# Kernel tuning notes

Hardware: AMD Instinct MI355X
Metric: run time of the kernel (lower is better)

Reference implementation:

```python
import jax, jax.numpy as jnp
import numpy as np
import math

N_EMBD = 1024
N_HEAD = 16
B, T, T_PLAN = 2, 2048, 512
EPS = 1e-5


def _layernorm(x, g, b):
    m = jnp.mean(x, axis=-1, keepdims=True)
    v = jnp.mean(jnp.square(x - m), axis=-1, keepdims=True)
    return (x - m) * jax.lax.rsqrt(v + EPS) * g + b


def setup_inputs() -> dict:
    key = jax.random.key(0)
    ks = jax.random.split(key, 16)
    C = N_EMBD
    s = 0.02
    inp = {
        "x": jax.random.normal(ks[0], (B, T, C), jnp.float32),
        "plan_hidden": jax.random.normal(ks[1], (B, T_PLAN, C), jnp.float32),
        "ln1_g": jnp.ones((C,), jnp.float32), "ln1_b": jnp.zeros((C,), jnp.float32),
        # weights stored as [in, out] (torch Linear applies x @ W.T)
        "c_attn_w": s * jax.random.normal(ks[2], (C, 3 * C), jnp.float32),
        "c_attn_b": jnp.zeros((3 * C,), jnp.float32),
        "attn_proj_w": s * jax.random.normal(ks[3], (C, C), jnp.float32),
        "attn_proj_b": jnp.zeros((C,), jnp.float32),
        "ln2_g": jnp.ones((C,), jnp.float32), "ln2_b": jnp.zeros((C,), jnp.float32),
        "q_w": s * jax.random.normal(ks[4], (C, C), jnp.float32), "q_b": jnp.zeros((C,), jnp.float32),
        "k_w": s * jax.random.normal(ks[5], (C, C), jnp.float32), "k_b": jnp.zeros((C,), jnp.float32),
        "v_w": s * jax.random.normal(ks[6], (C, C), jnp.float32), "v_b": jnp.zeros((C,), jnp.float32),
        "ca_proj_w": s * jax.random.normal(ks[7], (C, C), jnp.float32),
        "ca_proj_b": jnp.zeros((C,), jnp.float32),
        "ln3_g": jnp.ones((C,), jnp.float32), "ln3_b": jnp.zeros((C,), jnp.float32),
        "fc_w": s * jax.random.normal(ks[8], (C, 4 * C), jnp.float32),
        "fc_b": jnp.zeros((4 * C,), jnp.float32),
        "mlp_proj_w": s * jax.random.normal(ks[9], (4 * C, C), jnp.float32),
        "mlp_proj_b": jnp.zeros((C,), jnp.float32),
    }
    return inp


def _split_heads(t, n_head):  # [B,T,C] -> [B,H,T,D]
    Bs, Ts, Cs = t.shape
    return t.reshape(Bs, Ts, n_head, Cs // n_head).transpose(0, 2, 1, 3)


def _merge_heads(t):  # [B,H,T,D] -> [B,T,C]
    Bs, H, Ts, D = t.shape
    return t.transpose(0, 2, 1, 3).reshape(Bs, Ts, H * D)


def _self_attn(x, c_attn_w, c_attn_b, proj_w, proj_b):
    Bs, Ts, C = x.shape
    qkv = x @ c_attn_w + c_attn_b
    q, k, v = jnp.split(qkv, 3, axis=-1)
    q, k, v = (_split_heads(t, N_HEAD) for t in (q, k, v))
    scale = 1.0 / math.sqrt(C // N_HEAD)
    att = jnp.einsum("bhqd,bhkd->bhqk", q, k) * scale
    mask = jnp.tril(jnp.ones((Ts, Ts), bool))
    att = jnp.where(mask, att, -jnp.inf)
    att = jax.nn.softmax(att, axis=-1)
    y = jnp.einsum("bhqk,bhkd->bhqd", att, v)
    return _merge_heads(y) @ proj_w + proj_b


def _cross_attn(x, plan, q_w, q_b, k_w, k_b, v_w, v_b, proj_w, proj_b):
    C = x.shape[-1]
    q = _split_heads(x @ q_w + q_b, N_HEAD)
    k = _split_heads(plan @ k_w + k_b, N_HEAD)
    v = _split_heads(plan @ v_w + v_b, N_HEAD)
    scale = 1.0 / math.sqrt(C // N_HEAD)
    att = jax.nn.softmax(jnp.einsum("bhqd,bhkd->bhqk", q, k) * scale, axis=-1)
    y = jnp.einsum("bhqk,bhkd->bhqd", att, v)
    return _merge_heads(y) @ proj_w + proj_b


def reference(x, plan_hidden, ln1_g, ln1_b, c_attn_w, c_attn_b, attn_proj_w, attn_proj_b,
              ln2_g, ln2_b, q_w, q_b, k_w, k_b, v_w, v_b, ca_proj_w, ca_proj_b,
              ln3_g, ln3_b, fc_w, fc_b, mlp_proj_w, mlp_proj_b):
    x = x + _self_attn(_layernorm(x, ln1_g, ln1_b), c_attn_w, c_attn_b, attn_proj_w, attn_proj_b)
    x = x + _cross_attn(_layernorm(x, ln2_g, ln2_b), plan_hidden,
                        q_w, q_b, k_w, k_b, v_w, v_b, ca_proj_w, ca_proj_b)
    h = _layernorm(x, ln3_g, ln3_b)
    h = jax.nn.gelu(h @ fc_w + fc_b, approximate=False) @ mlp_proj_w + mlp_proj_b
    return x + h
```

## Files before the change

kernel.cpp:

```cpp
#include <hip/hip_runtime.h>
#include <stdint.h>

typedef __bf16 bf16;
typedef __bf16 bf16x4 __attribute__((ext_vector_type(4)));
typedef __bf16 bf16x8 __attribute__((ext_vector_type(8)));
typedef float  f32x4  __attribute__((ext_vector_type(4)));

#define DEVI __device__ __forceinline__

DEVI void gll16(const void* g, void* l) {
  __builtin_amdgcn_global_load_lds(
      (const __attribute__((address_space(1))) void*)g,
      (__attribute__((address_space(3))) void*)l,
      16, 0, 0);
}

DEVI f32x4 mfma16(bf16x8 a, bf16x8 b, f32x4 c) {
  return __builtin_amdgcn_mfma_f32_16x16x32_bf16(a, b, c, 0, 0, 0);
}

DEVI void wt_body(char* arena, const float* __restrict__ W, bf16* __restrict__ WT,
                  int K, int N, int bx, int by, int tid) {
  float (*t)[65] = reinterpret_cast<float(*)[65]>(arena);
  int bn = bx * 64, bk = by * 64;
  int tx = tid & 63, ty = tid >> 6;
#pragma unroll
  for (int i = 0; i < 16; ++i)
    t[ty + i * 4][tx] = W[(size_t)(bk + ty + i * 4) * N + bn + tx];
  __syncthreads();
#pragma unroll
  for (int i = 0; i < 16; ++i)
    WT[(size_t)(bn + ty + i * 4) * K + bk + tx] = (bf16)t[tx][ty + i * 4];
}

DEVI void ln_body(char* arena, const float* __restrict__ x, const float* __restrict__ g,
                  const float* __restrict__ b, bf16* __restrict__ out, int row, int tid) {
  float* ps  = (float*)arena;
  float* psq = ps + 4;
  f32x4 v = ((const f32x4*)(x + (size_t)row * 1024))[tid];
  float s = v[0] + v[1] + v[2] + v[3];
  float sq = v[0]*v[0] + v[1]*v[1] + v[2]*v[2] + v[3]*v[3];
#pragma unroll
  for (int m = 1; m < 64; m <<= 1) {
    s  += __shfl_xor(s, m, 64);
    sq += __shfl_xor(sq, m, 64);
  }
  int w = tid >> 6;
  if ((tid & 63) == 0) { ps[w] = s; psq[w] = sq; }
  __syncthreads();
  s  = ps[0] + ps[1] + ps[2] + ps[3];
  sq = psq[0] + psq[1] + psq[2] + psq[3];
  float mean = s * (1.f / 1024.f);
  float rs = rsqrtf(sq * (1.f / 1024.f) - mean * mean + 1e-5f);
  f32x4 gv = ((const f32x4*)g)[tid];
  f32x4 bv = ((const f32x4*)b)[tid];
  bf16x4 o;
#pragma unroll
  for (int i = 0; i < 4; ++i) o[i] = (bf16)((v[i] - mean) * rs * gv[i] + bv[i]);
  ((bf16x4*)(out + (size_t)row * 1024))[tid] = o;
}

__global__ __launch_bounds__(256)
void k_ln(const float* __restrict__ x, const float* __restrict__ g,
          const float* __restrict__ b, bf16* __restrict__ out) {
  __shared__ __align__(16) char arena[64];
  ln_body(arena, x, g, b, out, blockIdx.x, threadIdx.x);
}

__global__ __launch_bounds__(256)
void mega_misc(const float* __restrict__ x, const float* __restrict__ g,
               const float* __restrict__ b, bf16* __restrict__ out,
               const float* __restrict__ W, bf16* __restrict__ WT,
               const float* __restrict__ plan, bf16* __restrict__ planb,
               const float* __restrict__ kb, const float* __restrict__ vb,
               float* __restrict__ biaskv) {
  __shared__ __align__(16) char arena[16640];
  const int bid = blockIdx.x, tid = threadIdx.x;
  if (bid < 4096) {
    ln_body(arena, x, g, b, out, bid, tid);
  } else if (bid < 4864) {
    int wid = bid - 4096;
    wt_body(arena, W, WT, 1024, 3072, wid % 48, wid / 48, tid);
  } else if (bid < 5888) {
    int i = (bid - 4864) * 256 + tid;
    f32x4 v = ((const f32x4*)plan)[i];
    bf16x4 o;
    o[0] = (bf16)v[0]; o[1] = (bf16)v[1]; o[2] = (bf16)v[2]; o[3] = (bf16)v[3];
    ((bf16x4*)planb)[i] = o;
  } else {
    int i = (bid - 5888) * 256 + tid;
    biaskv[i] = i < 1024 ? kb[i] : vb[i - 1024];
  }
}

template <int EPI>
DEVI void gemm_s_body(char* arena, const bf16* __restrict__ A, const bf16* __restrict__ BT,
                      const float* __restrict__ bias, void* __restrict__ Cout,
                      int M, int N, int K, const float* __restrict__ Xres,
                      int nwg, int bid) {
  char (*SA)[8192]  = reinterpret_cast<char(*)[8192]>(arena);
  char (*SB)[16384] = reinterpret_cast<char(*)[16384]>(arena + 16384);
  const int tid = threadIdx.x;
  const int lane = tid & 63;
  const int w = tid >> 6;
  const int wr = w >> 1, wc = w & 1;
  const int lr = lane & 15, lg = lane >> 4;
  const int nk = K >> 6;

  const int q = nwg >> 3, r = nwg & 7;
  const int xcd = bid & 7, loc = bid >> 3;
  const int wg = (xcd < r ? xcd * (q + 1) : r * (q + 1) + (xcd - r) * q) + loc;
  const int gy = M >> 6;
  const int m0 = (wg % gy) << 6, n0 = (wg / gy) << 7;

  const int c8 = tid & 7;
  const int hrb = tid >> 3;
  auto stgA = [&](int buf, int ktc) {
#pragma unroll
    for (int i = 0; i < 2; ++i) {
      int hr = i * 32 + hrb;
      const bf16* s = A + (size_t)(m0 + hr) * K + ((size_t)ktc << 6) + ((c8 ^ (hr & 7)) << 3);
      gll16(s, &SA[buf][(i * 256 + tid) * 16]);
    }
  };
  auto stgB = [&](int buf, int ktc) {
#pragma unroll
    for (int i = 0; i < 4; ++i) {
      int hr = i * 32 + hrb;
      const bf16* s = BT + (size_t)(n0 + hr) * K + ((size_t)ktc << 6) + ((c8 ^ (hr & 7)) << 3);
      gll16(s, &SB[buf][(i * 256 + tid) * 16]);
    }
  };
  auto rdf = [&](const char* base, int rloc, int ks) -> bf16x8 {
    return *(const bf16x8*)(base + rloc * 128 + (((ks << 6) + (lg << 4)) ^ ((rloc & 7) << 4)));
  };

  f32x4 acc[2][4] = {};

  stgA(0, 0); stgB(0, 0);
  __syncthreads();
  for (int kt = 0; kt < nk; ++kt) {
    const int cur = kt & 1;
    if (kt + 1 < nk) { stgA(cur ^ 1, kt + 1); stgB(cur ^ 1, kt + 1); }
    bf16x8 af[2][2], bfr[4][2];
#pragma unroll
    for (int i = 0; i < 2; ++i)
#pragma unroll
      for (int ks = 0; ks < 2; ++ks)
        af[i][ks] = rdf(SA[cur], wr * 32 + i * 16 + lr, ks);
#pragma unroll
    for (int j = 0; j < 4; ++j)
#pragma unroll
      for (int ks = 0; ks < 2; ++ks)
        bfr[j][ks] = rdf(SB[cur], wc * 64 + j * 16 + lr, ks);
#pragma unroll
    for (int i = 0; i < 2; ++i)
#pragma unroll
      for (int j = 0; j < 4; ++j)
#pragma unroll
        for (int ks = 0; ks < 2; ++ks)
          acc[i][j] = mfma16(af[i][ks], bfr[j][ks], acc[i][j]);
    __syncthreads();
  }

  float* of = (float*)Cout;
  bf16*  ob = (bf16*)Cout;
#pragma unroll
  for (int j = 0; j < 4; ++j) {
    int gn = n0 + wc * 64 + j * 16 + lr;
    float bv = bias[gn];
#pragma unroll
    for (int i = 0; i < 2; ++i) {
      int gmb = m0 + wr * 32 + i * 16 + lg * 4;
#pragma unroll
      for (int rr = 0; rr < 4; ++rr) {
        size_t idx = (size_t)(gmb + rr) * N + gn;
        float v = acc[i][j][rr] + bv;
        if (EPI == 0) ob[idx] = (bf16)v;
        else if (EPI == 1) of[idx] += v;
        else if (EPI == 3) of[idx] = Xres[idx] + v;
        else {
          float ge = 0.5f * v * (1.f + erff(v * 0.70710678f));
          ob[idx] = (bf16)ge;
        }
      }
    }
  }
}

template <int EPI>
__global__ __launch_bounds__(256, 3)
void k_gemm_s(const bf16* __restrict__ A, const bf16* __restrict__ BT,
              const float* __restrict__ bias, void* __restrict__ Cout,
              int M, int N, int K, const float* __restrict__ Xres) {
  __shared__ __align__(16) char arena[49152];
  gemm_s_body<EPI>(arena, A, BT, bias, Cout, M, N, K, Xres, gridDim.x, blockIdx.x);
}

__global__ __launch_bounds__(256, 3)
void mega_gemmA2(const bf16* __restrict__ A, const bf16* __restrict__ BT,
                 const float* __restrict__ bias, void* __restrict__ Cout,
                 const float* __restrict__ Xres,
                 const float* __restrict__ qw, bf16* __restrict__ qwt,
                 const float* __restrict__ kw, bf16* __restrict__ kwt,
                 const float* __restrict__ vw, bf16* __restrict__ vwt) {
  __shared__ __align__(16) char arena[49152];
  if ((int)blockIdx.x < 512) {
    gemm_s_body<3>(arena, A, BT, bias, Cout, 4096, 1024, 1024, Xres, 512, blockIdx.x);
  } else {
    int wid = blockIdx.x - 512;
    const float* W = wid < 256 ? qw : (wid < 512 ? kw : vw);
    bf16* WT = wid < 256 ? qwt : (wid < 512 ? kwt : vwt);
    int sub = wid & 255;
    wt_body(arena, W, WT, 1024, 1024, sub & 15, sub >> 4, threadIdx.x);
  }
}

__global__ __launch_bounds__(256, 3)
void mega_gemmB2(const bf16* __restrict__ A, const bf16* __restrict__ BT,
                 const float* __restrict__ bias, void* __restrict__ Cout,
                 const float* __restrict__ mw, bf16* __restrict__ mwt) {
  __shared__ __align__(16) char arena[49152];
  if ((int)blockIdx.x < 512) {
    gemm_s_body<1>(arena, A, BT, bias, Cout, 4096, 1024, 1024, nullptr, 512, blockIdx.x);
  } else {
    int wid = blockIdx.x - 512;
    wt_body(arena, mw, mwt, 4096, 1024, wid & 15, wid >> 4, threadIdx.x);
  }
}

__global__ __launch_bounds__(256, 3)
void mega_gemmC2(const bf16* __restrict__ Aq, const bf16* __restrict__ qwt,
                 const float* __restrict__ qb, void* __restrict__ qxo,
                 const bf16* __restrict__ Ap, const bf16* __restrict__ kwt,
                 const float* __restrict__ bkv, void* __restrict__ kvo) {
  __shared__ __align__(16) char arena[49152];
  if ((int)blockIdx.x < 512) {
    gemm_s_body<0>(arena, Aq, qwt, qb, qxo, 4096, 1024, 1024, nullptr, 512, blockIdx.x);
  } else {
    gemm_s_body<0>(arena, Ap, kwt, bkv, kvo, 1024, 2048, 1024, nullptr, 256, blockIdx.x - 512);
  }
}

template <int EPI>
__global__ __launch_bounds__(512, 2)
void k_gemm8(const bf16* __restrict__ A, const bf16* __restrict__ BT,
             const float* __restrict__ bias, void* __restrict__ Cout,
             int M, int N, int K) {
  __shared__ __align__(16) char SA[2][2][16384];
  __shared__ __align__(16) char SB[2][2][16384];
  const int tid = threadIdx.x;
  const int lane = tid & 63;
  const int w = tid >> 6;
  const int wm = w >> 2, wn = w & 3;
  const int lr = lane & 15, lg = lane >> 4;
  const int nk = K >> 6;

  const int nwg = gridDim.x;
  const int q = nwg >> 3, r = nwg & 7;
  const int xcd = blockIdx.x & 7, loc = blockIdx.x >> 3;
  const int wg = (xcd < r ? xcd * (q + 1) : r * (q + 1) + (xcd - r) * q) + loc;
  const int gy = M >> 8;
  const int m0 = (wg % gy) << 8, n0 = (wg / gy) << 8;

  const int c8 = tid & 7;
  auto stg = [&](char* dst, const bf16* src0, int base0, int half, int ktc) {
#pragma unroll
    for (int i = 0; i < 2; ++i) {
      int hr = i * 64 + (tid >> 3);
      const bf16* s = src0 + (size_t)(base0 + half * 128 + hr) * K + ((size_t)ktc << 6)
                    + ((c8 ^ (hr & 7)) << 3);
      gll16(s, dst + (i * 512 + tid) * 16);
    }
  };
  auto rdf = [&](const char* hbase, int rloc, int ks) -> bf16x8 {
    return *(const bf16x8*)(hbase + rloc * 128 + (((ks << 6) + (lg << 4)) ^ ((rloc & 7) << 4)));
  };

  f32x4 acc[8][4] = {};
  bf16x8 af[4][2], b0f[2][2], b1f[2][2];

  stg(SA[0][0], A, m0, 0, 0);
  stg(SB[0][0], BT, n0, 0, 0);
  stg(SB[0][1], BT, n0, 1, 0);
  stg(SA[0][1], A, m0, 1, 0);
  stg(SA[1][0], A, m0, 0, 1);
  stg(SB[1][0], BT, n0, 0, 1);
  asm volatile("s_waitcnt vmcnt(8)" ::: "memory");
  __builtin_amdgcn_s_barrier();

  for (int kt = 0; kt < nk; ++kt) {
    const int cur = kt & 1;
    const char* hA0 = SA[cur][0]; const char* hA1 = SA[cur][1];
    const char* hB0 = SB[cur][0]; const char* hB1 = SB[cur][1];
    const int tn  = (kt + 1 < nk) ? kt + 1 : nk - 1;
    const int tn2 = (kt + 2 < nk) ? kt + 2 : nk - 1;

    stg(SB[(kt + 1) & 1][1], BT, n0, 1, tn);
    asm volatile("s_waitcnt vmcnt(8)" ::: "memory");
#pragma unroll
    for (int i = 0; i < 4; ++i) {
      int rl = i * 32 + wm * 16 + lr;
#pragma unroll
      for (int ks = 0; ks < 2; ++ks) af[i][ks] = rdf(hA0, rl, ks);
    }
#pragma unroll
    for (int j = 0; j < 2; ++j) {
      int rl = j * 64 + wn * 16 + lr;
#pragma unroll
      for (int ks = 0; ks < 2; ++ks) b0f[j][ks] = rdf(hB0, rl, ks);
    }
    __builtin_amdgcn_s_barrier();
    __builtin_amdgcn_s_setprio(1);
#pragma unroll
    for (int i = 0; i < 4; ++i)
#pragma unroll
      for (int j = 0; j < 2; ++j)
#pragma unroll
        for (int ks = 0; ks < 2; ++ks)
          acc[i][j] = mfma16(af[i][ks], b0f[j][ks], acc[i][j]);
    __builtin_amdgcn_s_setprio(0);

    stg(SA[(kt + 1) & 1][1], A, m0, 1, tn);
    asm volatile("s_waitcnt vmcnt(8)" ::: "memory");
#pragma unroll
    for (int j = 0; j < 2; ++j) {
      int rl = j * 64 + wn * 16 + lr;
#pragma unroll
      for (int ks = 0; ks < 2; ++ks) b1f[j][ks] = rdf(hB1, rl, ks);
    }
    __builtin_amdgcn_s_barrier();
    __builtin_amdgcn_s_setprio(1);
#pragma unroll
    for (int i = 0; i < 4; ++i)
#pragma unroll
      for (int j = 0; j < 2; ++j)
#pragma unroll
        for (int ks = 0; ks < 2; ++ks)
          acc[i][2 + j] = mfma16(af[i][ks], b1f[j][ks], acc[i][2 + j]);
    __builtin_amdgcn_s_setprio(0);

    stg(SA[cur][0], A, m0, 0, tn2);
#pragma unroll
    for (int i = 0; i < 4; ++i) {
      int rl = i * 32 + wm * 16 + lr;
#pragma unroll
      for (int ks = 0; ks < 2; ++ks) af[i][ks] = rdf(hA1, rl, ks);
    }
    __builtin_amdgcn_s_barrier();
    __builtin_amdgcn_s_setprio(1);
#pragma unroll
    for (int i = 0; i < 4; ++i)
#pragma unroll
      for (int j = 0; j < 2; ++j)
#pragma unroll
        for (int ks = 0; ks < 2; ++ks)
          acc[4 + i][j] = mfma16(af[i][ks], b0f[j][ks], acc[4 + i][j]);
    __builtin_amdgcn_s_setprio(0);

    stg(SB[cur][0], BT, n0, 0, tn2);
    asm volatile("s_waitcnt vmcnt(8)" ::: "memory");
    __builtin_amdgcn_s_barrier();
    __builtin_amdgcn_s_setprio(1);
#pragma unroll
    for (int i = 0; i < 4; ++i)
#pragma unroll
      for (int j = 0; j < 2; ++j)
#pragma unroll
        for (int ks = 0; ks < 2; ++ks)
          acc[4 + i][2 + j] = mfma16(af[i][ks], b1f[j][ks], acc[4 + i][2 + j]);
    __builtin_amdgcn_s_setprio(0);
  }

  float* of = (float*)Cout;
  bf16*  ob = (bf16*)Cout;
#pragma unroll
  for (int ni = 0; ni < 4; ++ni) {
    int gn = n0 + (ni >> 1) * 128 + (ni & 1) * 64 + wn * 16 + lr;
    float bv = bias[gn];
#pragma unroll
    for (int mi = 0; mi < 8; ++mi) {
      int gmb = m0 + (mi >> 2) * 128 + (mi & 3) * 32 + wm * 16 + lg * 4;
#pragma unroll
      for (int rr = 0; rr < 4; ++rr) {
        size_t idx = (size_t)(gmb + rr) * N + gn;
        float v = acc[mi][ni][rr] + bv;
        if (EPI == 0) ob[idx] = (bf16)v;
        else if (EPI == 1) of[idx] += v;
        else {
          float ge = 0.5f * v * (1.f + erff(v * 0.70710678f));
          ob[idx] = (bf16)ge;
        }
      }
    }
  }
}

template <bool CAUSAL>
DEVI void attn_body(char* arena, int id,
                    const bf16* __restrict__ Qb, int ldq, int qcol0,
                    const bf16* __restrict__ Kb, int kcol0,
                    const bf16* __restrict__ Vb, int vcol0,
                    int ldkv, int qlen, int kvlen,
                    bf16* __restrict__ Ob, int ldo, float scale) {
  char (*Klds)[8192]   = reinterpret_cast<char(*)[8192]>(arena);
  bf16 (*VT)[64][68]   = reinterpret_cast<bf16(*)[64][68]>(arena + 16384);
  const int tid = threadIdx.x;
  const int lane = tid & 63;
  const int w = tid >> 6;
  const int lr = lane & 15, lg = lane >> 4;

  int h, b, qt;
  if (CAUSAL) {
    int low = id & 255;
    h = low & 15; b = (low >> 4) & 1;
    int q3 = low >> 5;
    qt = (id >> 8) ? (8 + q3) : (7 - q3);
  } else {
    h = id & 15; b = (id >> 4) & 1; qt = id >> 5;
  }

  const int qbase = qt * 128;
  const int kvbase = b * kvlen;
  const int nkv = CAUSAL ? (2 * qt + 2) : (kvlen >> 6);
  const int mask_from = CAUSAL ? (nkv - 2) : 0x7fffffff;

  bf16x8 qf[2][2];
#pragma unroll
  for (int g = 0; g < 2; ++g)
#pragma unroll
    for (int kk = 0; kk < 2; ++kk)
      qf[g][kk] = *(const bf16x8*)(Qb + (size_t)(b * qlen + qbase + w * 32 + g * 16 + lr) * ldq
                                   + qcol0 + h * 64 + kk * 32 + lg * 8);

  f32x4 o[2][4] = {};
  float mrun[2] = {-3.0e38f, -3.0e38f};
  float lsum[2] = {0.f, 0.f};

  bf16x8 vr0, vr1;
  const int vkv = lane;
  const int vd0 = (tid >> 6) * 16;
  const bf16* Vbase = Vb + vcol0 + h * 64 + vd0;

  auto stageK = [&](int buf, int kvt) {
#pragma unroll
    for (int t = 0; t < 2; ++t) {
      int r = t * 32 + (tid >> 3);
      int pb = (tid & 7) * 16;
      const char* gs = (const char*)(Kb + (size_t)(kvbase + kvt * 64 + r) * ldkv + kcol0 + h * 64)
                       + (pb ^ ((r & 7) << 4));
      gll16(gs, &Klds[buf][t * 4096 + tid * 16]);
    }
  };
  auto loadV = [&](int kvt) {
    const bf16* vp = Vbase + (size_t)(kvbase + kvt * 64 + vkv) * ldkv;
    vr0 = *(const bf16x8*)vp;
    vr1 = *(const bf16x8*)(vp + 8);
  };
  auto writeV = [&](int buf) {
#pragma unroll
    for (int i = 0; i < 8; ++i) VT[buf][vd0 + i][vkv] = vr0[i];
#pragma unroll
    for (int i = 0; i < 8; ++i) VT[buf][vd0 + 8 + i][vkv] = vr1[i];
  };

  stageK(0, 0);
  loadV(0);
  writeV(0);
  __syncthreads();

  int cur = 0;
  for (int kvt = 0; kvt < nkv; ++kvt) {
    if (kvt + 1 < nkv) { stageK(cur ^ 1, kvt + 1); loadV(kvt + 1); }

    f32x4 s[2][4] = {};
#pragma unroll
    for (int sub = 0; sub < 4; ++sub) {
      int row = sub * 16 + lr;
#pragma unroll
      for (int kk = 0; kk < 2; ++kk) {
        bf16x8 kf = *(const bf16x8*)&Klds[cur][(row << 7) + ((kk * 64 + lg * 16) ^ ((row & 7) << 4))];
        s[0][sub] = mfma16(kf, qf[0][kk], s[0][sub]);
        s[1][sub] = mfma16(kf, qf[1][kk], s[1][sub]);
      }
    }

    const bool domask = CAUSAL && (kvt >= mask_from);
    bf16x8 pa[2][2];
#pragma unroll
    for (int g = 0; g < 2; ++g) {
      const int qg = qbase + w * 32 + g * 16 + lr;
      float pmax = -3.0e38f;
#pragma unroll
      for (int sub = 0; sub < 4; ++sub)
#pragma unroll
        for (int j = 0; j < 4; ++j) {
          float v = s[g][sub][j] * scale;
          if (domask) {
            int kvg = kvt * 64 + sub * 16 + lg * 4 + j;
            if (kvg > qg) v = -3.0e38f;
          }
          s[g][sub][j] = v;
          pmax = fmaxf(pmax, v);
        }
      pmax = fmaxf(pmax, __shfl_xor(pmax, 16, 64));
      pmax = fmaxf(pmax, __shfl_xor(pmax, 32, 64));
      float mnew = mrun[g];
      if (__any(pmax - mrun[g] > 8.f)) {
        mnew = fmaxf(mrun[g], pmax);
        float alpha = __expf(mrun[g] - mnew);
        lsum[g] *= alpha;
        float al[4];
#pragma unroll
        for (int j = 0; j < 4; ++j) {
          int src = (lane & 48) | (lg * 4 + j);
          al[j] = __int_as_float(__builtin_amdgcn_ds_bpermute(src << 2, __float_as_int(alpha)));
        }
#pragma unroll
        for (int dt = 0; dt < 4; ++dt)
#pragma unroll
          for (int j = 0; j < 4; ++j) o[g][dt][j] *= al[j];
      }
      float psum = 0.f;
#pragma unroll
      for (int sub = 0; sub < 4; ++sub)
#pragma unroll
        for (int j = 0; j < 4; ++j) {
          float p = __expf(s[g][sub][j] - mnew);
          s[g][sub][j] = p;
          psum += p;
        }
      psum += __shfl_xor(psum, 16, 64);
      psum += __shfl_xor(psum, 32, 64);
      lsum[g] += psum;
      mrun[g] = mnew;
#pragma unroll
      for (int sp = 0; sp < 2; ++sp) {
#pragma unroll
        for (int j = 0; j < 4; ++j) {
          pa[g][sp][j]     = (bf16)s[g][2 * sp][j];
          pa[g][sp][4 + j] = (bf16)s[g][2 * sp + 1][j];
        }
      }
    }

#pragma unroll
    for (int sp = 0; sp < 2; ++sp) {
#pragma unroll
      for (int dt = 0; dt < 4; ++dt) {
        int d = dt * 16 + lr;
        bf16x4 va  = *(const bf16x4*)&VT[cur][d][sp * 32 + lg * 4];
        bf16x4 vb2 = *(const bf16x4*)&VT[cur][d][sp * 32 + 16 + lg * 4];
        bf16x8 vf = __builtin_shufflevector(va, vb2, 0, 1, 2, 3, 4, 5, 6, 7);
        o[0][dt] = mfma16(pa[0][sp], vf, o[0][dt]);
        o[1][dt] = mfma16(pa[1][sp], vf, o[1][dt]);
      }
    }

    if (kvt + 1 < nkv) writeV(cur ^ 1);
    __syncthreads();
    cur ^= 1;
  }

#pragma unroll
  for (int g = 0; g < 2; ++g) {
    float il[4];
#pragma unroll
    for (int j = 0; j < 4; ++j) {
      int src = (lane & 48) | (lg * 4 + j);
      float ls = __int_as_float(__builtin_amdgcn_ds_bpermute(src << 2, __float_as_int(lsum[g])));
      il[j] = 1.0f / ls;
    }
#pragma unroll
    for (int dt = 0; dt < 4; ++dt)
#pragma unroll
      for (int j = 0; j < 4; ++j) {
        int gq = b * qlen + qbase + w * 32 + g * 16 + lg * 4 + j;
        Ob[(size_t)gq * ldo + h * 64 + dt * 16 + lr] = (bf16)(o[g][dt][j] * il[j]);
      }
  }
}

template <bool CAUSAL, bool WT2>
__global__ __launch_bounds__(256)
void mega_attn_wt(const bf16* __restrict__ Qb, int ldq, int qcol0,
                  const bf16* __restrict__ Kb, int kcol0,
                  const bf16* __restrict__ Vb, int vcol0,
                  int ldkv, int qlen, int kvlen,
                  bf16* __restrict__ Ob, int ldo, float scale,
                  const float* __restrict__ W1, bf16* __restrict__ WT1,
                  const float* __restrict__ W2, bf16* __restrict__ WT2b) {
  __shared__ __align__(16) char arena[33792];
  if ((int)blockIdx.x < 512) {
    attn_body<CAUSAL>(arena, blockIdx.x, Qb, ldq, qcol0, Kb, kcol0, Vb, vcol0,
                      ldkv, qlen, kvlen, Ob, ldo, scale);
  } else if ((int)blockIdx.x < 768) {
    int wid = blockIdx.x - 512;
    wt_body(arena, W1, WT1, 1024, 1024, wid & 15, wid >> 4, threadIdx.x);
  } else if (WT2) {
    int wid = blockIdx.x - 768;
    wt_body(arena, W2, WT2b, 1024, 4096, wid & 63, wid >> 6, threadIdx.x);
  }
}

extern "C" void kernel_launch(void* const* d_in, const int* in_sizes, int n_in,
                              void* d_out, int out_size, void* d_ws, size_t ws_size,
                              hipStream_t stream) {
  (void)in_sizes; (void)n_in; (void)out_size; (void)ws_size;
  const float* x        = (const float*)d_in[0];
  const float* plan     = (const float*)d_in[1];
  const float* ln1_g    = (const float*)d_in[2];
  const float* ln1_b    = (const float*)d_in[3];
  const float* c_attn_w = (const float*)d_in[4];
  const float* c_attn_b = (const float*)d_in[5];
  const float* aproj_w  = (const float*)d_in[6];
  const float* aproj_b  = (const float*)d_in[7];
  const float* ln2_g    = (const float*)d_in[8];
  const float* ln2_b    = (const float*)d_in[9];
  const float* q_w      = (const float*)d_in[10];
  const float* q_b      = (const float*)d_in[11];
  const float* k_w      = (const float*)d_in[12];
  const float* k_b      = (const float*)d_in[13];
  const float* v_w      = (const float*)d_in[14];
  const float* v_b      = (const float*)d_in[15];
  const float* ca_w     = (const float*)d_in[16];
  const float* ca_b     = (const float*)d_in[17];
  const float* ln3_g    = (const float*)d_in[18];
  const float* ln3_b    = (const float*)d_in[19];
  const float* fc_w     = (const float*)d_in[20];
  const float* fc_b     = (const float*)d_in[21];
  const float* mp_w     = (const float*)d_in[22];
  const float* mp_b     = (const float*)d_in[23];

  char* ws = (char*)d_ws;
  bf16*  wbuf   = (bf16*)(ws);
  bf16*  lnb    = (bf16*)(ws + (8ull << 20));
  bf16*  planb  = (bf16*)(ws + (16ull << 20));
  bf16*  yb     = (bf16*)(ws + (18ull << 20));
  char*  rega   = ws + (26ull << 20);
  float* biaskv = (float*)(ws + (58ull << 20));
  bf16* qkv  = (bf16*)rega;
  bf16* qwt  = (bf16*)rega;
  bf16* kwt  = (bf16*)(rega + (2ull << 20));
  bf16* kvc  = (bf16*)(rega + (8ull << 20));
  bf16* co   = (bf16*)(rega + (12ull << 20));
  bf16* hmid = (bf16*)rega;
  bf16* aprojT = lnb;
  bf16* caT    = lnb;
  bf16* fcT    = wbuf;
  bf16* mpT    = yb;
  float* xw = (float*)d_out;

  mega_misc<<<5896, 256, 0, stream>>>(x, ln1_g, ln1_b, lnb, c_attn_w, wbuf,
                                      plan, planb, k_b, v_b, biaskv);
  k_gemm8<0><<<192, 512, 0, stream>>>(lnb, wbuf, c_attn_b, qkv, 4096, 3072, 1024);
  mega_attn_wt<true, true><<<512 + 256 + 1024, 256, 0, stream>>>(
      qkv, 3072, 0, qkv, 1024, qkv, 2048, 3072, 2048, 2048, yb, 1024, 0.125f,
      aproj_w, aprojT, fc_w, fcT);
  mega_gemmA2<<<512 + 768, 256, 0, stream>>>(yb, aprojT, aproj_b, xw, x,
                                             q_w, qwt, k_w, kwt, v_w, kwt + (1u << 20));
  k_ln<<<4096, 256, 0, stream>>>(xw, ln2_g, ln2_b, lnb);
  mega_gemmC2<<<768, 256, 0, stream>>>(lnb, qwt, q_b, yb, planb, kwt, biaskv, kvc);
  mega_attn_wt<false, false><<<512 + 256, 256, 0, stream>>>(
      yb, 1024, 0, kvc, 0, kvc, 1024, 2048, 2048, 512, co, 1024, 0.125f,
      ca_w, caT, nullptr, nullptr);
  mega_gemmB2<<<512 + 1024, 256, 0, stream>>>(co, caT, ca_b, xw, mp_w, mpT);
  k_ln<<<4096, 256, 0, stream>>>(xw, ln3_g, ln3_b, lnb);
  k_gemm8<2><<<256, 512, 0, stream>>>(lnb, fcT, fc_b, hmid, 4096, 4096, 1024);
  k_gemm_s<1><<<512, 256, 0, stream>>>(hmid, mpT, mp_b, xw, 4096, 1024, 4096, nullptr);
}
```

Before: 295.8 us.

## Move cross-attn K/V projection earlier and transpose K/V weights in first kernel

The K/V weight transposes move into the first misc kernel. The plan K/V projection GEMM moves from the post-LN2 kernel into the attention-projection kernel, since it depends only on plan_hidden. The Q projection then runs as a standalone GEMM. Workspace buffers are reshuffled so kvc, qwt, caT and kwt no longer alias live data. The aim is better load balance, filling the attention-proj GEMM wave with independent work and shortening the critical-path Q GEMM, at the cost of a longer first kernel and more workspace usage.

Result: no change. 297.7 us (+0.7%).

```diff
diff --git a/kernel.cpp b/kernel.cpp
--- a/kernel.cpp
+++ b/kernel.cpp
@@ -73,7 +73,9 @@
                const float* __restrict__ W, bf16* __restrict__ WT,
                const float* __restrict__ plan, bf16* __restrict__ planb,
                const float* __restrict__ kb, const float* __restrict__ vb,
-               float* __restrict__ biaskv) {
+               float* __restrict__ biaskv,
+               const float* __restrict__ kw, bf16* __restrict__ kwt,
+               const float* __restrict__ vw, bf16* __restrict__ vwt) {
   __shared__ __align__(16) char arena[16640];
   const int bid = blockIdx.x, tid = threadIdx.x;
   if (bid < 4096) {
@@ -87,9 +89,15 @@
     bf16x4 o;
     o[0] = (bf16)v[0]; o[1] = (bf16)v[1]; o[2] = (bf16)v[2]; o[3] = (bf16)v[3];
     ((bf16x4*)planb)[i] = o;
-  } else {
+  } else if (bid < 5896) {
     int i = (bid - 5888) * 256 + tid;
     biaskv[i] = i < 1024 ? kb[i] : vb[i - 1024];
+  } else if (bid < 6152) {
+    int wid = bid - 5896;
+    wt_body(arena, kw, kwt, 1024, 1024, wid & 15, wid >> 4, tid);
+  } else {
+    int wid = bid - 6152;
+    wt_body(arena, vw, vwt, 1024, 1024, wid & 15, wid >> 4, tid);
   }
 }
 
@@ -198,21 +206,20 @@
 }
 
 __global__ __launch_bounds__(256, 3)
-void mega_gemmA2(const bf16* __restrict__ A, const bf16* __restrict__ BT,
+void mega_gemmA3(const bf16* __restrict__ A, const bf16* __restrict__ BT,
                  const float* __restrict__ bias, void* __restrict__ Cout,
                  const float* __restrict__ Xres,
-                 const float* __restrict__ qw, bf16* __restrict__ qwt,
-                 const float* __restrict__ kw, bf16* __restrict__ kwt,
-                 const float* __restrict__ vw, bf16* __restrict__ vwt) {
+                 const bf16* __restrict__ Ap, const bf16* __restrict__ kvwt,
+                 const float* __restrict__ bkv, void* __restrict__ kvo,
+                 const float* __restrict__ qw, bf16* __restrict__ qwt) {
   __shared__ __align__(16) char arena[49152];
   if ((int)blockIdx.x < 512) {
     gemm_s_body<3>(arena, A, BT, bias, Cout, 4096, 1024, 1024, Xres, 512, blockIdx.x);
+  } else if ((int)blockIdx.x < 768) {
+    gemm_s_body<0>(arena, Ap, kvwt, bkv, kvo, 1024, 2048, 1024, nullptr, 256, blockIdx.x - 512);
   } else {
-    int wid = blockIdx.x - 512;
-    const float* W = wid < 256 ? qw : (wid < 512 ? kw : vw);
-    bf16* WT = wid < 256 ? qwt : (wid < 512 ? kwt : vwt);
-    int sub = wid & 255;
-    wt_body(arena, W, WT, 1024, 1024, sub & 15, sub >> 4, threadIdx.x);
+    int wid = blockIdx.x - 768;
+    wt_body(arena, qw, qwt, 1024, 1024, wid & 15, wid >> 4, threadIdx.x);
   }
 }
 
@@ -226,19 +233,6 @@
   } else {
     int wid = blockIdx.x - 512;
     wt_body(arena, mw, mwt, 4096, 1024, wid & 15, wid >> 4, threadIdx.x);
-  }
-}
-
-__global__ __launch_bounds__(256, 3)
-void mega_gemmC2(const bf16* __restrict__ Aq, const bf16* __restrict__ qwt,
-                 const float* __restrict__ qb, void* __restrict__ qxo,
-                 const bf16* __restrict__ Ap, const bf16* __restrict__ kwt,
-                 const float* __restrict__ bkv, void* __restrict__ kvo) {
-  __shared__ __align__(16) char arena[49152];
-  if ((int)blockIdx.x < 512) {
-    gemm_s_body<0>(arena, Aq, qwt, qb, qxo, 4096, 1024, 1024, nullptr, 512, blockIdx.x);
-  } else {
-    gemm_s_body<0>(arena, Ap, kwt, bkv, kvo, 1024, 2048, 1024, nullptr, 256, blockIdx.x - 512);
   }
 }
 
@@ -639,28 +633,29 @@
   bf16*  yb     = (bf16*)(ws + (18ull << 20));
   char*  rega   = ws + (26ull << 20);
   float* biaskv = (float*)(ws + (58ull << 20));
-  bf16* qkv  = (bf16*)rega;
-  bf16* qwt  = (bf16*)rega;
-  bf16* kwt  = (bf16*)(rega + (2ull << 20));
-  bf16* kvc  = (bf16*)(rega + (8ull << 20));
-  bf16* co   = (bf16*)(rega + (12ull << 20));
-  bf16* hmid = (bf16*)rega;
+  bf16* qkv    = (bf16*)rega;
+  bf16* kvc    = (bf16*)rega;
+  bf16* qwt    = (bf16*)(rega + (4ull << 20));
+  bf16* caT    = (bf16*)(rega + (4ull << 20));
+  bf16* co     = (bf16*)(rega + (8ull << 20));
+  bf16* kwt    = (bf16*)(rega + (24ull << 20));
+  bf16* hmid   = (bf16*)rega;
   bf16* aprojT = lnb;
-  bf16* caT    = lnb;
   bf16* fcT    = wbuf;
   bf16* mpT    = yb;
   float* xw = (float*)d_out;
 
-  mega_misc<<<5896, 256, 0, stream>>>(x, ln1_g, ln1_b, lnb, c_attn_w, wbuf,
-                                      plan, planb, k_b, v_b, biaskv);
+  mega_misc<<<6408, 256, 0, stream>>>(x, ln1_g, ln1_b, lnb, c_attn_w, wbuf,
+                                      plan, planb, k_b, v_b, biaskv,
+                                      k_w, kwt, v_w, kwt + (1u << 20));
   k_gemm8<0><<<192, 512, 0, stream>>>(lnb, wbuf, c_attn_b, qkv, 4096, 3072, 1024);
   mega_attn_wt<true, true><<<512 + 256 + 1024, 256, 0, stream>>>(
       qkv, 3072, 0, qkv, 1024, qkv, 2048, 3072, 2048, 2048, yb, 1024, 0.125f,
       aproj_w, aprojT, fc_w, fcT);
-  mega_gemmA2<<<512 + 768, 256, 0, stream>>>(yb, aprojT, aproj_b, xw, x,
-                                             q_w, qwt, k_w, kwt, v_w, kwt + (1u << 20));
+  mega_gemmA3<<<512 + 256 + 256, 256, 0, stream>>>(yb, aprojT, aproj_b, xw, x,
+                                                   planb, kwt, biaskv, kvc, q_w, qwt);
   k_ln<<<4096, 256, 0, stream>>>(xw, ln2_g, ln2_b, lnb);
-  mega_gemmC2<<<768, 256, 0, stream>>>(lnb, qwt, q_b, yb, planb, kwt, biaskv, kvc);
+  k_gemm_s<0><<<512, 256, 0, stream>>>(lnb, qwt, q_b, yb, 4096, 1024, 1024, nullptr);
   mega_attn_wt<false, false><<<512 + 256, 256, 0, stream>>>(
       yb, 1024, 0, kvc, 0, kvc, 1024, 2048, 2048, 512, co, 1024, 0.125f,
       ca_w, caT, nullptr, nullptr);
```
